# Kernel optimization log

Measured on AMD Instinct MI355X. Metric: run time of the kernel, lower is better.

The kernel has to match this reference:

```python
import jax, jax.numpy as jnp
import numpy as np

D_MODEL = 768
D_STATE = 128
D_CONV = 4
EXPAND = 4
D_INNER = EXPAND * D_MODEL  # 3072
DT_RANK = 48  # ceil(768/16), mamba default dt_rank='auto'
H_MLP = 768
EPS = 1e-6


def setup_inputs() -> dict:
    key = jax.random.key(0)
    ks = jax.random.split(key, 12)
    B, T = 1, 384

    def rn(k, shape, s=0.02):
        return jax.random.normal(k, shape, jnp.float32) * s

    inp = {}
    inp["x"] = jax.random.normal(ks[0], (B, 3 * T, D_MODEL), jnp.float32)
    inp["ln_w"] = jnp.ones((6, D_MODEL), jnp.float32)  # ln1..ln6 RMSNorm weights
    # 3 independent Mamba blocks, params stacked on leading dim
    inp["in_proj_w"] = rn(ks[1], (3, 2 * D_INNER, D_MODEL))
    inp["conv_w"] = rn(ks[2], (3, D_INNER, 1, D_CONV), 0.1)  # depthwise causal conv1d
    inp["conv_b"] = rn(ks[3], (3, D_INNER), 0.1)
    inp["x_proj_w"] = rn(ks[4], (3, DT_RANK + 2 * D_STATE, D_INNER))
    inp["dt_proj_w"] = rn(ks[5], (3, D_INNER, DT_RANK), 0.1)
    inp["dt_proj_b"] = rn(ks[6], (3, D_INNER), 0.1) - 4.0  # small dt after softplus
    A = jnp.tile(jnp.arange(1, D_STATE + 1, dtype=jnp.float32)[None, None, :], (3, D_INNER, 1))
    inp["A_log"] = jnp.log(A)  # mamba S4D-real init
    inp["D_skip"] = jnp.ones((3, D_INNER), jnp.float32)
    inp["out_proj_w"] = rn(ks[7], (3, D_MODEL, D_INNER))
    # 3 GatedMLPs: fc1 -> 2*hidden (value, gate), silu gate, fc2 -> out
    inp["fc1_w"] = rn(ks[8], (3, 2 * H_MLP, D_MODEL))
    inp["fc1_b"] = jnp.zeros((3, 2 * H_MLP), jnp.float32)
    inp["fc2_w"] = rn(ks[9], (3, D_MODEL, H_MLP))
    inp["fc2_b"] = jnp.zeros((3, D_MODEL), jnp.float32)
    return inp


def _rmsnorm(x, w):
    v = jnp.mean(jnp.square(x), axis=-1, keepdims=True)
    return x * jax.lax.rsqrt(v + EPS) * w


def _mamba(u, in_w, cw, cb, xp_w, dt_w, dt_b, A_log, D_skip, out_w):
    # u: (B, T, D_MODEL)
    Bsz = u.shape[0]
    xz = u @ in_w.T  # (B,T,2*Di)
    x, z = jnp.split(xz, 2, axis=-1)
    # causal depthwise conv1d over time
    xc = jax.lax.conv_general_dilated(
        jnp.swapaxes(x, 1, 2), cw, (1,), [(D_CONV - 1, 0)],
        feature_group_count=D_INNER)  # (B,Di,T)
    x = jax.nn.silu(jnp.swapaxes(xc, 1, 2) + cb)  # (B,T,Di)
    x_dbl = x @ xp_w.T  # (B,T,dt_rank+2N)
    dt = x_dbl[..., :DT_RANK]
    Bm = x_dbl[..., DT_RANK:DT_RANK + D_STATE]
    Cm = x_dbl[..., DT_RANK + D_STATE:]
    delta = jax.nn.softplus(dt @ dt_w.T + dt_b)  # (B,T,Di)
    A = -jnp.exp(A_log)  # (Di,N)

    def step(h, inp):
        d_t, B_t, C_t, u_t = inp  # (B,Di),(B,N),(B,N),(B,Di)
        h = jnp.exp(d_t[:, :, None] * A) * h + (d_t * u_t)[:, :, None] * B_t[:, None, :]
        y = jnp.einsum('bdn,bn->bd', h, C_t)
        return h, y

    h0 = jnp.zeros((Bsz, D_INNER, D_STATE), u.dtype)
    xs = tuple(jnp.swapaxes(a, 0, 1) for a in (delta, Bm, Cm, x))  # time-major
    _, ys = jax.lax.scan(jax.checkpoint(step), h0, xs)
    y = jnp.swapaxes(ys, 0, 1) + x * D_skip  # (B,T,Di)
    return (y * jax.nn.silu(z)) @ out_w.T  # (B,T,D_MODEL)


def _gmlp(x, w1, b1, w2, b2):
    h = x @ w1.T + b1
    a, g = jnp.split(h, 2, axis=-1)
    return (jax.nn.silu(g) * a) @ w2.T + b2


def reference(x, ln_w, in_proj_w, conv_w, conv_b, x_proj_w, dt_proj_w, dt_proj_b,
              A_log, D_skip, out_proj_w, fc1_w, fc1_b, fc2_w, fc2_b):
    t = x.shape[1] // 3
    outs = []
    for i in range(3):  # music / up / down branches
        b = x[:, i * t:(i + 1) * t]
        b = b + _mamba(_rmsnorm(b, ln_w[2 * i]), in_proj_w[i], conv_w[i], conv_b[i],
                       x_proj_w[i], dt_proj_w[i], dt_proj_b[i], A_log[i], D_skip[i],
                       out_proj_w[i])
        b = b + _gmlp(_rmsnorm(b, ln_w[2 * i + 1]), fc1_w[i], fc1_b[i], fc2_w[i], fc2_b[i])
        outs.append(b)
    return jnp.concatenate(outs, axis=1)
```

## Files before the change

### kernel.cpp

```cpp
#include <hip/hip_runtime.h>
#include <hip/hip_bf16.h>

#define TSEQ 384
#define DMODEL 768
#define DINNER 3072
#define DSTATE 128
#define DTRANK 48
#define XPROJ_N (DTRANK + 2*DSTATE)
#define NSEG 3
#define LOG2E 1.44269504088896340736f
#define LN2F  0.69314718055994530942f

typedef __attribute__((ext_vector_type(8))) short short8;
typedef __attribute__((ext_vector_type(4))) float floatx4;
typedef unsigned short u16;
typedef unsigned int u32;

__device__ __forceinline__ float bf2f(u16 u) {
    return __uint_as_float(((unsigned)u) << 16);
}
__device__ __forceinline__ float ldf(const void* p, size_t i, int bf) {
    return bf ? bf2f(((const u16*)p)[i]) : ((const float*)p)[i];
}
__device__ __forceinline__ void stf(void* p, size_t i, float v, int bf) {
    if (bf) ((__hip_bfloat16*)p)[i] = __float2bfloat16(v);
    else    ((float*)p)[i] = v;
}
__device__ __forceinline__ float silu_f(float v) { return v / (1.f + __expf(-v)); }
__device__ __forceinline__ u16 f2bf(float f) {
    unsigned u = __float_as_uint(f);
    return (u16)((u + 0x7FFFu + ((u >> 16) & 1u)) >> 16);
}

__device__ __forceinline__ float exp2_fast(float x) {
#if __has_builtin(__builtin_amdgcn_exp2f)
    return __builtin_amdgcn_exp2f(x);
#else
    return exp2f(x);
#endif
}

template<int CTRL>
__device__ __forceinline__ float ror_add(float x) {
    int r = __builtin_amdgcn_update_dpp(0, __float_as_int(x), CTRL, 0xF, 0xF, true);
    return x + __int_as_float(r);
}

__device__ __forceinline__ void gl16(const void* g, void* l) {
    __builtin_amdgcn_global_load_lds(
        (const __attribute__((address_space(1))) u32*)g,
        (__attribute__((address_space(3))) u32*)l, 16, 0, 0);
}

__global__ void k_detect(const unsigned* lnw_bits, int* flag) {
    if (threadIdx.x == 0) {
        flag[0] = (lnw_bits[0] == 0x3F803F80u) ? 1 : 0;
    }
}

__global__ __launch_bounds__(256) void k_rmsnorm(
    const void* src, int src_is_f32, const void* lnw, int wbase,
    u16* out, const int* flagp)
{
    int bf  = *flagp;
    int sbf = src_is_f32 ? 0 : bf;
    int r   = blockIdx.x;
    int seg = r / TSEQ;
    int wrow = 2*seg + wbase;
    int tid = threadIdx.x;
    float v[3]; float s = 0.f;
    #pragma unroll
    for (int j = 0; j < 3; ++j) {
        int e = j*256 + tid;
        v[j] = ldf(src, (size_t)r*DMODEL + e, sbf);
        s += v[j]*v[j];
    }
    __shared__ float red[256];
    red[tid] = s; __syncthreads();
    for (int st = 128; st > 0; st >>= 1) {
        if (tid < st) red[tid] += red[tid+st];
        __syncthreads();
    }
    float rs = rsqrtf(red[0]/(float)DMODEL + 1e-6f);
    #pragma unroll
    for (int j = 0; j < 3; ++j) {
        int e = j*256 + tid;
        out[(size_t)r*DMODEL + e] = f2bf(v[j]*rs*ldf(lnw, (size_t)wrow*DMODEL + e, bf));
    }
}

__global__ __launch_bounds__(256) void k_gemm(
    const float* A, const void* W, const void* bias,
    float* C, const int* flagp, int M, int N, int K, int lda)
{
    int bf  = *flagp;
    int seg = blockIdx.z;
    int mbase = blockIdx.y * 64, nbase = blockIdx.x * 64;
    int tid = threadIdx.x;
    int tx = tid & 15, ty = tid >> 4;

    __shared__ float As[16][68];
    __shared__ float Ws[16][68];

    const float* Ag = A + (size_t)seg*M*lda;
    size_t segW = (size_t)seg*N*K;

    int lrow = tid >> 2;
    int lk   = (tid & 3) * 4;
    int wn   = nbase + lrow;

    float acc[4][4];
    #pragma unroll
    for (int i = 0; i < 4; ++i)
        #pragma unroll
        for (int j = 0; j < 4; ++j) acc[i][j] = 0.f;

    for (int kt = 0; kt < K; kt += 16) {
        float4 av = *reinterpret_cast<const float4*>(Ag + (size_t)(mbase+lrow)*lda + kt + lk);
        As[lk+0][lrow] = av.x; As[lk+1][lrow] = av.y;
        As[lk+2][lrow] = av.z; As[lk+3][lrow] = av.w;
        float w0=0.f, w1=0.f, w2=0.f, w3=0.f;
        if (wn < N) {
            size_t off = segW + (size_t)wn*K + kt + lk;
            if (bf) {
                ushort4 q = *reinterpret_cast<const ushort4*>((const u16*)W + off);
                w0 = bf2f(q.x); w1 = bf2f(q.y); w2 = bf2f(q.z); w3 = bf2f(q.w);
            } else {
                float4 f = *reinterpret_cast<const float4*>((const float*)W + off);
                w0 = f.x; w1 = f.y; w2 = f.z; w3 = f.w;
            }
        }
        Ws[lk+0][lrow] = w0; Ws[lk+1][lrow] = w1;
        Ws[lk+2][lrow] = w2; Ws[lk+3][lrow] = w3;
        __syncthreads();
        #pragma unroll
        for (int kk = 0; kk < 16; ++kk) {
            float4 a4 = *reinterpret_cast<const float4*>(&As[kk][ty*4]);
            float4 b4 = *reinterpret_cast<const float4*>(&Ws[kk][tx*4]);
            float ar[4] = {a4.x, a4.y, a4.z, a4.w};
            float br[4] = {b4.x, b4.y, b4.z, b4.w};
            #pragma unroll
            for (int i = 0; i < 4; ++i)
                #pragma unroll
                for (int j = 0; j < 4; ++j)
                    acc[i][j] = fmaf(ar[i], br[j], acc[i][j]);
        }
        __syncthreads();
    }

    #pragma unroll
    for (int i = 0; i < 4; ++i) {
        int m = mbase + ty*4 + i;
        #pragma unroll
        for (int j = 0; j < 4; ++j) {
            int n = nbase + tx*4 + j;
            if (n < N) {
                float v = acc[i][j] + ldf(bias, (size_t)seg*N + n, bf);
                v = (v > 20.f) ? v : log1pf(__expf(v));
                C[((size_t)(seg*M + m))*N + n] = v;
            }
        }
    }
}

__global__ __launch_bounds__(256) void k_gemm_mfma64g(
    const u16* A, const void* W, const void* bias, const void* resid,
    int resid_flagged, void* C, int c_mode, const int* flagp,
    int M, int N, int K, int ksplit)
{
    int bf  = *flagp;
    int zz  = blockIdx.z;
    int seg = zz / ksplit, ks = zz - seg*ksplit;
    int mbase = blockIdx.y * 64, nbase = blockIdx.x * 64;
    int tid = threadIdx.x;
    int w = tid >> 6, lane = tid & 63;
    int wm = w >> 1, wn = w & 1;
    int quad = lane >> 4, l16 = lane & 15;

    __shared__ short As[3][64*64];
    __shared__ short Ws[3][64*64];

    int nk = (K >> 6) / ksplit;
    size_t k0 = ((size_t)ks * nk) << 6;
    const u16* Ag = A + (size_t)seg*M*K + (size_t)mbase*K + k0;
    size_t segWK = (size_t)seg*N*K;

    int srow = lane >> 3;
    int scol = ((lane & 7) ^ srow) * 8;
    int swz  = (l16 & 7) * 8;

    floatx4 acc[2][2];
    #pragma unroll
    for (int i = 0; i < 2; ++i)
        #pragma unroll
        for (int j = 0; j < 2; ++j)
            acc[i][j] = (floatx4){0.f, 0.f, 0.f, 0.f};

    auto CMP = [&](int b) {
        #pragma unroll
        for (int kk = 0; kk < 2; ++kk) {
            short8 af[2], bfr[2];
            #pragma unroll
            for (int i = 0; i < 2; ++i) {
                int row = wm*32 + i*16 + l16;
                af[i] = *reinterpret_cast<const short8*>(
                    &As[b][row*64 + (((kk*4 + quad)*8) ^ swz)]);
            }
            #pragma unroll
            for (int j = 0; j < 2; ++j) {
                int row = wn*32 + j*16 + l16;
                bfr[j] = *reinterpret_cast<const short8*>(
                    &Ws[b][row*64 + (((kk*4 + quad)*8) ^ swz)]);
            }
            #pragma unroll
            for (int i = 0; i < 2; ++i)
                #pragma unroll
                for (int j = 0; j < 2; ++j)
                    acc[i][j] = __builtin_amdgcn_mfma_f32_16x16x32_bf16(af[i], bfr[j], acc[i][j], 0, 0, 0);
        }
    };

    if (bf) {
        const u16* Wb = (const u16*)W;
        auto STG = [&](int t, int b) {
            size_t kt = (size_t)t << 6;
            #pragma unroll
            for (int i8 = 0; i8 < 2; ++i8) {
                int rbase = w*16 + i8*8;
                gl16(Ag + (size_t)(rbase + srow)*K + kt + scol, &As[b][rbase*64]);
                int wr = nbase + rbase + srow;
                if (wr > N - 1) wr = N - 1;
                gl16(Wb + segWK + (size_t)wr*K + k0 + kt + scol, &Ws[b][rbase*64]);
            }
        };
        STG(0, 0);
        STG(1, 1);
        for (int t = 0; t < nk - 2; ++t) {
            STG(t + 2, (t + 2) % 3);
            asm volatile("s_waitcnt vmcnt(8)" ::: "memory");
            __builtin_amdgcn_s_barrier();
            __builtin_amdgcn_sched_barrier(0);
            CMP(t % 3);
            asm volatile("" ::: "memory");
            __builtin_amdgcn_s_barrier();
        }
        asm volatile("s_waitcnt vmcnt(4)" ::: "memory");
        __builtin_amdgcn_s_barrier();
        __builtin_amdgcn_sched_barrier(0);
        CMP((nk - 2) % 3);
        asm volatile("" ::: "memory");
        __builtin_amdgcn_s_barrier();
        asm volatile("s_waitcnt vmcnt(0)" ::: "memory");
        __builtin_amdgcn_s_barrier();
        __builtin_amdgcn_sched_barrier(0);
        CMP((nk - 1) % 3);
    } else {
        const float* Wf = (const float*)W + segWK;
        int row2 = tid >> 2;
        int wr2 = nbase + row2; if (wr2 > N - 1) wr2 = N - 1;
        for (int t = 0; t < nk; ++t) {
            size_t kt = (size_t)t << 6;
            #pragma unroll
            for (int i8 = 0; i8 < 2; ++i8) {
                int rbase = w*16 + i8*8;
                gl16(Ag + (size_t)(rbase + srow)*K + kt + scol, &As[0][rbase*64]);
            }
            const float* wp = Wf + (size_t)wr2*K + k0 + kt;
            #pragma unroll
            for (int h2 = 0; h2 < 2; ++h2) {
                int gs = (tid & 3) + h2*4;
                short8 s;
                #pragma unroll
                for (int q2 = 0; q2 < 8; ++q2) s[q2] = (short)f2bf(wp[gs*8 + q2]);
                *reinterpret_cast<short8*>(&Ws[0][row2*64 + ((gs ^ (row2 & 7)) * 8)]) = s;
            }
            __syncthreads();
            CMP(0);
            __syncthreads();
        }
    }

    #pragma unroll
    for (int i = 0; i < 2; ++i) {
        #pragma unroll
        for (int reg = 0; reg < 4; ++reg) {
            int grow = mbase + wm*32 + i*16 + quad*4 + reg;
            #pragma unroll
            for (int j = 0; j < 2; ++j) {
                int gcol = nbase + wn*32 + j*16 + l16;
                if (gcol < N) {
                    float v = acc[i][j][reg];
                    size_t idx = ((size_t)(seg*M + grow))*N + gcol;
                    if (ksplit == 1) {
                        if (bias) v += ldf(bias, (size_t)seg*N + gcol, bf);
                        if (resid) v += resid_flagged ? ldf(resid, idx, bf)
                                                      : ((const float*)resid)[idx];
                        if      (c_mode == 0) ((float*)C)[idx] = v;
                        else if (c_mode == 1) ((u16*)C)[idx] = f2bf(v);
                        else                  stf(C, idx, v, bf);
                    } else {
                        if (ks == 0) {
                            if (bias)  v += ldf(bias, (size_t)seg*N + gcol, bf);
                            if (resid) v += resid_flagged ? ldf(resid, idx, bf)
                                                          : ((const float*)resid)[idx];
                        }
                        atomicAdd(&((float*)C)[idx], v);
                    }
                }
            }
        }
    }
}

__global__ __launch_bounds__(256) void k_fc1_gate_g(
    const u16* A, const void* W, const void* bias, u16* act, const int* flagp)
{
    const int M = TSEQ, K = DMODEL, NF = 2*DMODEL;
    int bf  = *flagp;
    int seg = blockIdx.z;
    int mbase = blockIdx.y * 64, nbase = blockIdx.x * 64;
    int tid = threadIdx.x;
    int w = tid >> 6, lane = tid & 63;
    int wm = w >> 1, wn = w & 1;
    int quad = lane >> 4, l16 = lane & 15;

    __shared__ short As[2][64*64];
    __shared__ short Wa[2][64*64];
    __shared__ short Wg[2][64*64];

    const u16* Ag  = A + (size_t)seg*M*K + (size_t)mbase*K;
    const u16* Wap = (const u16*)W + (size_t)seg*NF*K + (size_t)nbase*K;
    const u16* Wgp = Wap + (size_t)DMODEL*K;
    int nk = K >> 6;

    int srow = lane >> 3;
    int scol = ((lane & 7) ^ srow) * 8;
    int swz  = (l16 & 7) * 8;

    floatx4 acca[2][2], accg[2][2];
    #pragma unroll
    for (int i = 0; i < 2; ++i)
        #pragma unroll
        for (int j = 0; j < 2; ++j) {
            acca[i][j] = (floatx4){0.f, 0.f, 0.f, 0.f};
            accg[i][j] = (floatx4){0.f, 0.f, 0.f, 0.f};
        }

    auto CMP = [&](int b) {
        #pragma unroll
        for (int kk = 0; kk < 2; ++kk) {
            short8 af[2], ba[2], bg[2];
            #pragma unroll
            for (int i = 0; i < 2; ++i) {
                int row = wm*32 + i*16 + l16;
                af[i] = *reinterpret_cast<const short8*>(
                    &As[b][row*64 + (((kk*4 + quad)*8) ^ swz)]);
            }
            #pragma unroll
            for (int j = 0; j < 2; ++j) {
                int row = wn*32 + j*16 + l16;
                int col = ((kk*4 + quad)*8) ^ swz;
                ba[j] = *reinterpret_cast<const short8*>(&Wa[b][row*64 + col]);
                bg[j] = *reinterpret_cast<const short8*>(&Wg[b][row*64 + col]);
            }
            #pragma unroll
            for (int i = 0; i < 2; ++i)
                #pragma unroll
                for (int j = 0; j < 2; ++j) {
                    acca[i][j] = __builtin_amdgcn_mfma_f32_16x16x32_bf16(af[i], ba[j], acca[i][j], 0, 0, 0);
                    accg[i][j] = __builtin_amdgcn_mfma_f32_16x16x32_bf16(af[i], bg[j], accg[i][j], 0, 0, 0);
                }
        }
    };

    if (bf) {
        auto STG = [&](int t, int b) {
            size_t kt = (size_t)t << 6;
            #pragma unroll
            for (int i8 = 0; i8 < 2; ++i8) {
                int rbase = w*16 + i8*8;
                size_t so = (size_t)(rbase + srow)*K + kt + scol;
                gl16(Ag  + so, &As[b][rbase*64]);
                gl16(Wap + so, &Wa[b][rbase*64]);
                gl16(Wgp + so, &Wg[b][rbase*64]);
            }
        };
        STG(0, 0);
        for (int t = 0; t < nk - 1; ++t) {
            STG(t + 1, (t + 1) & 1);
            asm volatile("s_waitcnt vmcnt(6)" ::: "memory");
            __builtin_amdgcn_s_barrier();
            __builtin_amdgcn_sched_barrier(0);
            CMP(t & 1);
            asm volatile("" ::: "memory");
            __builtin_amdgcn_s_barrier();
        }
        asm volatile("s_waitcnt vmcnt(0)" ::: "memory");
        __builtin_amdgcn_s_barrier();
        __builtin_amdgcn_sched_barrier(0);
        CMP((nk - 1) & 1);
    } else {
        const float* Waf = (const float*)W + (size_t)seg*NF*K + (size_t)nbase*K;
        const float* Wgf = Waf + (size_t)DMODEL*K;
        int row2 = tid >> 2;
        for (int t = 0; t < nk; ++t) {
            size_t kt = (size_t)t << 6;
            #pragma unroll
            for (int i8 = 0; i8 < 2; ++i8) {
                int rbase = w*16 + i8*8;
                gl16(Ag + (size_t)(rbase + srow)*K + kt + scol, &As[0][rbase*64]);
            }
            #pragma unroll
            for (int h2 = 0; h2 < 2; ++h2) {
                int gs = (tid & 3) + h2*4;
                int wcol = (gs ^ (row2 & 7)) * 8;
                short8 sa, sg;
                const float* wpa = Waf + (size_t)row2*K + kt + gs*8;
                const float* wpg = Wgf + (size_t)row2*K + kt + gs*8;
                #pragma unroll
                for (int q2 = 0; q2 < 8; ++q2) { sa[q2] = (short)f2bf(wpa[q2]); sg[q2] = (short)f2bf(wpg[q2]); }
                *reinterpret_cast<short8*>(&Wa[0][row2*64 + wcol]) = sa;
                *reinterpret_cast<short8*>(&Wg[0][row2*64 + wcol]) = sg;
            }
            __syncthreads();
            CMP(0);
            __syncthreads();
        }
    }

    #pragma unroll
    for (int i = 0; i < 2; ++i) {
        #pragma unroll
        for (int reg = 0; reg < 4; ++reg) {
            int grow = mbase + wm*32 + i*16 + quad*4 + reg;
            #pragma unroll
            for (int j = 0; j < 2; ++j) {
                int gcol = nbase + wn*32 + j*16 + l16;
                float va = acca[i][j][reg] + ldf(bias, (size_t)seg*NF + gcol, bf);
                float vg = accg[i][j][reg] + ldf(bias, (size_t)seg*NF + DMODEL + gcol, bf);
                act[((size_t)(seg*M + grow))*DMODEL + gcol] = f2bf(va * silu_f(vg));
            }
        }
    }
}

__global__ __launch_bounds__(256) void k_conv(
    const u16* xz, const void* cw, const void* cb, u16* xconv, const int* flagp)
{
    int bf = *flagp;
    size_t gid = ((size_t)blockIdx.x*256 + threadIdx.x) * 8;
    int d = (int)(gid % DINNER);
    size_t rt = gid / DINNER;
    int t = (int)(rt % TSEQ);
    int seg = (int)(rt / TSEQ);

    float wv[4][8];
    if (bf) {
        const u16* cwp = (const u16*)cw + ((size_t)seg*DINNER + d)*4;
        #pragma unroll
        for (int q = 0; q < 4; ++q) {
            short8 s = *reinterpret_cast<const short8*>(cwp + q*8);
            #pragma unroll
            for (int e = 0; e < 8; ++e) {
                int idx = q*8 + e;
                wv[idx & 3][idx >> 2] = bf2f((u16)s[e]);
            }
        }
    } else {
        const float* cwp = (const float*)cw + ((size_t)seg*DINNER + d)*4;
        #pragma unroll
        for (int idx = 0; idx < 32; ++idx)
            wv[idx & 3][idx >> 2] = cwp[idx];
    }

    float acc[8];
    #pragma unroll
    for (int e = 0; e < 8; ++e) acc[e] = ldf(cb, (size_t)seg*DINNER + d + e, bf);

    const u16* xs = xz + (size_t)seg*TSEQ*(2*DINNER) + d;
    #pragma unroll
    for (int j = 0; j < 4; ++j) {
        int ts = t - 3 + j;
        if (ts >= 0) {
            short8 v = *reinterpret_cast<const short8*>(xs + (size_t)ts*(2*DINNER));
            #pragma unroll
            for (int e = 0; e < 8; ++e)
                acc[e] = fmaf(wv[j][e], bf2f((u16)v[e]), acc[e]);
        }
    }
    short8 o;
    #pragma unroll
    for (int e = 0; e < 8; ++e) o[e] = (short)f2bf(silu_f(acc[e]));
    *reinterpret_cast<short8*>(xconv + gid) = o;
}

#define WSCH 4
#define WSCT 8
#define NPAIR (TSEQ/(2*WSCT))
#define NBX   (DINNER/WSCH)
#define GUARD_TH 0.04f

__global__ __launch_bounds__(64) void k_scan_wave(
    const float* delta, const u16* xconv, const float* xdbl, const u16* xz,
    const void* A_log, const void* D_skip, u16* yout, const int* flagp)
{
    int bf   = flagp[0];
    int seg  = blockIdx.y;
    int bx = (int)blockIdx.x;
    bx = (bx & 7) * (NBX/8) + (bx >> 3);
    int dbase = bx * WSCH;
    int lane = threadIdx.x;
    int ch = lane >> 4, sl = lane & 15;
    int d = dbase + ch;

    __shared__ float4 BUF[2][WSCT][64];
    __shared__ float  DLB2[WSCT][8];

    float a[8];
    size_t abase = ((size_t)seg*DINNER + d)*DSTATE + (size_t)sl*8;
    #pragma unroll
    for (int j = 0; j < 8; ++j)
        a[j] = -__expf(ldf(A_log, abase + j, bf)) * LOG2E;
    float gl[8]; float gmax = 0.f;
    gl[0] = 0.f;
    #pragma unroll
    for (int j = 1; j < 8; ++j) {
        gl[j] = (a[j] - a[j-1]) * LN2F;
        gmax = fmaxf(gmax, fabsf(gl[j]));
    }
    float wg = gmax;
    #pragma unroll
    for (int k = 32; k >= 1; k >>= 1) wg = fmaxf(wg, __shfl_xor(wg, k));
    float a0  = a[0];
    float Dsk = ldf(D_skip, (size_t)seg*DINNER + d, bf);
    float dskg = (sl == 0) ? Dsk : 0.f;

    const float* xdbl_s = xdbl + (size_t)seg*TSEQ*XPROJ_N;
    int loff = DTRANK + (lane & 15)*8 + ((lane >> 4) & 1)*4 + ((lane >> 5) ? DSTATE : 0);
    const float* srcl = xdbl_s + loff;

    const float* delta_s = delta + (size_t)seg*TSEQ*DINNER + dbase;
    const u16*   xconv_s = xconv + (size_t)seg*TSEQ*DINNER + dbase;
    const u16*   z_s     = xz    + (size_t)seg*TSEQ*(2*DINNER) + DINNER + dbase + ch;
    u16*         y_s     = yout  + (size_t)seg*TSEQ*DINNER + dbase + ch;

    float4  pdel = (float4){0.f, 0.f, 0.f, 0.f};
    ushort4 pu   = (ushort4){0, 0, 0, 0};
    u16     pz   = 0;

    auto STAGE = [&](int tile, int buf) {
        const float* rb = srcl + (size_t)tile*WSCT*XPROJ_N;
        #pragma unroll
        for (int t = 0; t < WSCT; ++t)
            gl16(rb + (size_t)t*XPROJ_N, &BUF[buf][t][0]);
    };
    auto PLOAD = [&](int tile) {
        if (lane < WSCT) {
            size_t ro = (size_t)(tile*WSCT + lane)*DINNER;
            pdel = *reinterpret_cast<const float4*>(delta_s + ro);
            pu   = *reinterpret_cast<const ushort4*>(xconv_s + ro);
        }
    };
    auto DSTORE = [&]() -> bool {
        if (lane < WSCT) {
            float4 w0 = (float4){pdel.x, bf2f(pu.x), pdel.y, bf2f(pu.y)};
            float4 w1 = (float4){pdel.z, bf2f(pu.z), pdel.w, bf2f(pu.w)};
            *reinterpret_cast<float4*>(&DLB2[lane][0]) = w0;
            *reinterpret_cast<float4*>(&DLB2[lane][4]) = w1;
        }
        float m4 = fmaxf(fmaxf(pdel.x, pdel.y), fmaxf(pdel.z, pdel.w));
        return __any(m4 * wg > GUARD_TH);
    };

    float h[8];
    #pragma unroll
    for (int j = 0; j < 8; ++j) h[j] = 0.f;
    float yr = 0.f;

    float2 duA, duB, duC;
    float4 b0A, b1A, c0A, c1A;
    float4 b0B, b1B, c0B, c1B;
    float4 b0C, b1C, c0C, c1C;

#define LOADOPS(BP, T, S) do {                                                \
    du##S = *reinterpret_cast<const float2*>(&DLB2[T][ch*2]);                 \
    b0##S = (BP)[(T)*64 + sl];                                                \
    b1##S = (BP)[(T)*64 + 16 + sl];                                           \
    c0##S = (BP)[(T)*64 + 32 + sl];                                           \
    c1##S = (BP)[(T)*64 + 48 + sl];                                           \
} while (0)

#define COMPUTE(S, T) do {                                                    \
    float del = du##S.x, ut = du##S.y;                                        \
    float duu = del * ut;                                                     \
    float e0,e1,e2,e3,e4,e5,e6,e7;                                            \
    if (gf) {                                                                 \
        e0 = exp2_fast(del * a0);                                             \
        e1 = e0 * fmaf(del, gl[1], 1.f);                                      \
        e2 = e1 * fmaf(del, gl[2], 1.f);                                      \
        e3 = e2 * fmaf(del, gl[3], 1.f);                                      \
        e4 = e3 * fmaf(del, gl[4], 1.f);                                      \
        e5 = e4 * fmaf(del, gl[5], 1.f);                                      \
        e6 = e5 * fmaf(del, gl[6], 1.f);                                      \
        e7 = e6 * fmaf(del, gl[7], 1.f);                                      \
    } else {                                                                  \
        e0 = exp2_fast(del*a[0]); e1 = exp2_fast(del*a[1]);                   \
        e2 = exp2_fast(del*a[2]); e3 = exp2_fast(del*a[3]);                   \
        e4 = exp2_fast(del*a[4]); e5 = exp2_fast(del*a[5]);                   \
        e6 = exp2_fast(del*a[6]); e7 = exp2_fast(del*a[7]);                   \
    }                                                                         \
    h[0] = fmaf(e0, h[0], duu*b0##S.x);                                       \
    h[1] = fmaf(e1, h[1], duu*b0##S.y);                                       \
    h[2] = fmaf(e2, h[2], duu*b0##S.z);                                       \
    h[3] = fmaf(e3, h[3], duu*b0##S.w);                                       \
    h[4] = fmaf(e4, h[4], duu*b1##S.x);                                       \
    h[5] = fmaf(e5, h[5], duu*b1##S.y);                                       \
    h[6] = fmaf(e6, h[6], duu*b1##S.z);                                       \
    h[7] = fmaf(e7, h[7], duu*b1##S.w);                                       \
    float p0 = ut * dskg;                                                     \
    p0 = fmaf(h[0], c0##S.x, p0);                                             \
    p0 = fmaf(h[1], c0##S.y, p0);                                             \
    p0 = fmaf(h[2], c0##S.z, p0);                                             \
    p0 = fmaf(h[3], c0##S.w, p0);                                             \
    float p1 = h[4]*c1##S.x;                                                  \
    p1 = fmaf(h[5], c1##S.y, p1);                                             \
    p1 = fmaf(h[6], c1##S.z, p1);                                             \
    p1 = fmaf(h[7], c1##S.w, p1);                                             \
    float p = p0 + p1;                                                        \
    p = ror_add<0x128>(p);                                                    \
    p = ror_add<0x124>(p);                                                    \
    p = ror_add<0x122>(p);                                                    \
    p = ror_add<0x121>(p);                                                    \
    if (sl == (half8 | (T))) yr = p;                                          \
} while (0)

    auto do_tile = [&](const float4* bp, bool gf, int half8) {
        LOADOPS(bp, 0, A);
        LOADOPS(bp, 1, B);
        LOADOPS(bp, 2, C);
        COMPUTE(A, 0);
        LOADOPS(bp, 3, A);
        COMPUTE(B, 1);
        LOADOPS(bp, 4, B);
        COMPUTE(C, 2);
        LOADOPS(bp, 5, C);
        COMPUTE(A, 3);
        LOADOPS(bp, 6, A);
        COMPUTE(B, 4);
        LOADOPS(bp, 7, B);
        COMPUTE(C, 5);
        COMPUTE(A, 6);
        COMPUTE(B, 7);
    };

    STAGE(0, 0);
    PLOAD(0);

    for (int p = 0; p < NPAIR; ++p) {
        int tA = 2*p;
        asm volatile("s_waitcnt vmcnt(0)" ::: "memory");
        bool exA = DSTORE();
        STAGE(tA + 1, 1);
        PLOAD(tA + 1);
        pz = z_s[(size_t)(p*16 + sl) * (size_t)(2*DINNER)];
        __builtin_amdgcn_sched_barrier(0);
        do_tile(&BUF[0][0][0], !exA, 0);
        asm volatile("s_waitcnt vmcnt(0)" ::: "memory");
        bool exB = DSTORE();
        if (tA + 2 < 2*NPAIR) {
            STAGE(tA + 2, 0);
            PLOAD(tA + 2);
        }
        __builtin_amdgcn_sched_barrier(0);
        do_tile(&BUF[1][0][0], !exB, 8);
        y_s[(size_t)(p*16 + sl) * (size_t)DINNER] = f2bf(yr * silu_f(bf2f(pz)));
        yr = 0.f;
    }
#undef LOADOPS
#undef COMPUTE
}

extern "C" void kernel_launch(void* const* d_in, const int* in_sizes, int n_in,
                              void* d_out, int out_size, void* d_ws, size_t ws_size,
                              hipStream_t stream) {
    const void* x     = d_in[0];
    const void* lnw   = d_in[1];
    const void* inw   = d_in[2];
    const void* convw = d_in[3];
    const void* convb = d_in[4];
    const void* xpw   = d_in[5];
    const void* dtw   = d_in[6];
    const void* dtb   = d_in[7];
    const void* alog  = d_in[8];
    const void* dsk   = d_in[9];
    const void* outw  = d_in[10];
    const void* fc1w  = d_in[11];
    const void* fc1b  = d_in[12];
    const void* fc2w  = d_in[13];
    const void* fc2b  = d_in[14];

    int* flag = (int*)d_ws;
    char* wsb = (char*)d_ws;
    const size_t N_U    = (size_t)NSEG*TSEQ*DMODEL;
    const size_t N_XZ   = (size_t)NSEG*TSEQ*2*DINNER;
    const size_t N_XC   = (size_t)NSEG*TSEQ*DINNER;
    const size_t N_XDBL = (size_t)NSEG*TSEQ*XPROJ_N;

    u16*   u     = (u16*)(wsb + 16);
    u16*   xz    = u + N_U;
    u16*   xconv = xz + N_XZ;
    float* xdbl  = (float*)(xconv + N_XC);
    float* delta = xdbl + N_XDBL;
    u16*   yfin  = (u16*)(delta + N_XC);
    float* b1    = (float*)(yfin + N_XC);
    u16*   actb  = (u16*)(b1 + N_U);

    k_detect<<<1, 64, 0, stream>>>((const unsigned*)lnw, flag);
    hipMemsetAsync(xdbl, 0, N_XDBL*sizeof(float), stream);
    hipMemsetAsync(b1,   0, N_U*sizeof(float),   stream);

    k_rmsnorm<<<NSEG*TSEQ, 256, 0, stream>>>(x, 0, lnw, 0, u, flag);
    k_gemm_mfma64g<<<dim3(96, 6, NSEG), 256, 0, stream>>>(u, inw, nullptr, nullptr, 0,
        xz, 1, flag, TSEQ, 2*DINNER, DMODEL, 1);
    k_conv<<<(NSEG*TSEQ*DINNER)/(256*8), 256, 0, stream>>>(xz, convw, convb, xconv, flag);
    k_gemm_mfma64g<<<dim3(5, 6, NSEG*4), 256, 0, stream>>>(xconv, xpw, nullptr, nullptr, 0,
        xdbl, 0, flag, TSEQ, XPROJ_N, DINNER, 4);
    k_gemm<<<dim3(48, 6, NSEG), 256, 0, stream>>>(xdbl, dtw, dtb,
        delta, flag, TSEQ, DINNER, DTRANK, XPROJ_N);

    k_scan_wave<<<dim3(NBX, NSEG), 64, 0, stream>>>(
        delta, xconv, xdbl, xz, alog, dsk, yfin, flag);

    k_gemm_mfma64g<<<dim3(12, 6, NSEG*4), 256, 0, stream>>>(yfin, outw, nullptr, x, 1,
        b1, 0, flag, TSEQ, DMODEL, DINNER, 4);

    k_rmsnorm<<<NSEG*TSEQ, 256, 0, stream>>>(b1, 1, lnw, 1, u, flag);
    k_fc1_gate_g<<<dim3(12, 6, NSEG), 256, 0, stream>>>(u, fc1w, fc1b, actb, flag);
    k_gemm_mfma64g<<<dim3(12, 6, NSEG), 256, 0, stream>>>(actb, fc2w, fc2b, b1, 0,
        d_out, 2, flag, TSEQ, DMODEL, DMODEL, 1);
}
```

Baseline: 496.0 us.

## Split scan wave over 2 channels with 4 states per lane and swizzle reduction

The selective-scan wave kernel now handles 2 channels per 64-lane wave instead of 4. Each lane owns 4 states instead of 8, over 4-step time tiles. The per-step cross-lane reduction grows from 4 DPP row-rotate adds to 5 ds_swizzle adds spanning 32 lanes. This shortens each lane's serial per-step work and doubles the number of waves, at the cost of more blocks, a longer reduction built on LDS-path swizzles, and more sync points per sequence.

Result: slower. 522.5 us (+5.4%).

```diff
diff --git a/kernel.cpp b/kernel.cpp
--- a/kernel.cpp
+++ b/kernel.cpp
@@ -40,9 +40,9 @@
 #endif
 }
 
-template<int CTRL>
-__device__ __forceinline__ float ror_add(float x) {
-    int r = __builtin_amdgcn_update_dpp(0, __float_as_int(x), CTRL, 0xF, 0xF, true);
+template<int MASK>
+__device__ __forceinline__ float swz_add(float x) {
+    int r = __builtin_amdgcn_ds_swizzle(__float_as_int(x), MASK);
     return x + __int_as_float(r);
 }
 
@@ -494,8 +494,8 @@
     *reinterpret_cast<short8*>(xconv + gid) = o;
 }
 
-#define WSCH 4
-#define WSCT 8
+#define WSCH 2
+#define WSCT 4
 #define NPAIR (TSEQ/(2*WSCT))
 #define NBX   (DINNER/WSCH)
 #define GUARD_TH 0.04f
@@ -510,21 +510,22 @@
     bx = (bx & 7) * (NBX/8) + (bx >> 3);
     int dbase = bx * WSCH;
     int lane = threadIdx.x;
-    int ch = lane >> 4, sl = lane & 15;
+    int ch = lane >> 5, sl = lane & 31;
     int d = dbase + ch;
+    int bq = (sl & 1)*16 + (sl >> 1);
 
     __shared__ float4 BUF[2][WSCT][64];
-    __shared__ float  DLB2[WSCT][8];
-
-    float a[8];
-    size_t abase = ((size_t)seg*DINNER + d)*DSTATE + (size_t)sl*8;
-    #pragma unroll
-    for (int j = 0; j < 8; ++j)
+    __shared__ float  DLB2[WSCT][4];
+
+    float a[4];
+    size_t abase = ((size_t)seg*DINNER + d)*DSTATE + (size_t)sl*4;
+    #pragma unroll
+    for (int j = 0; j < 4; ++j)
         a[j] = -__expf(ldf(A_log, abase + j, bf)) * LOG2E;
-    float gl[8]; float gmax = 0.f;
+    float gl[4]; float gmax = 0.f;
     gl[0] = 0.f;
     #pragma unroll
-    for (int j = 1; j < 8; ++j) {
+    for (int j = 1; j < 4; ++j) {
         gl[j] = (a[j] - a[j-1]) * LN2F;
         gmax = fmaxf(gmax, fabsf(gl[j]));
     }
@@ -544,9 +545,9 @@
     const u16*   z_s     = xz    + (size_t)seg*TSEQ*(2*DINNER) + DINNER + dbase + ch;
     u16*         y_s     = yout  + (size_t)seg*TSEQ*DINNER + dbase + ch;
 
-    float4  pdel = (float4){0.f, 0.f, 0.f, 0.f};
-    ushort4 pu   = (ushort4){0, 0, 0, 0};
-    u16     pz   = 0;
+    float2 pdel2 = (float2){0.f, 0.f};
+    u32    pu2   = 0;
+    u16    pz    = 0;
 
     auto STAGE = [&](int tile, int buf) {
         const float* rb = srcl + (size_t)tile*WSCT*XPROJ_N;
@@ -557,100 +558,72 @@
     auto PLOAD = [&](int tile) {
         if (lane < WSCT) {
             size_t ro = (size_t)(tile*WSCT + lane)*DINNER;
-            pdel = *reinterpret_cast<const float4*>(delta_s + ro);
-            pu   = *reinterpret_cast<const ushort4*>(xconv_s + ro);
+            pdel2 = *reinterpret_cast<const float2*>(delta_s + ro);
+            pu2   = *reinterpret_cast<const u32*>(xconv_s + ro);
         }
     };
     auto DSTORE = [&]() -> bool {
         if (lane < WSCT) {
-            float4 w0 = (float4){pdel.x, bf2f(pu.x), pdel.y, bf2f(pu.y)};
-            float4 w1 = (float4){pdel.z, bf2f(pu.z), pdel.w, bf2f(pu.w)};
+            float4 w0 = (float4){pdel2.x, bf2f((u16)(pu2 & 0xFFFFu)),
+                                 pdel2.y, bf2f((u16)(pu2 >> 16))};
             *reinterpret_cast<float4*>(&DLB2[lane][0]) = w0;
-            *reinterpret_cast<float4*>(&DLB2[lane][4]) = w1;
-        }
-        float m4 = fmaxf(fmaxf(pdel.x, pdel.y), fmaxf(pdel.z, pdel.w));
-        return __any(m4 * wg > GUARD_TH);
+        }
+        float m2 = fmaxf(pdel2.x, pdel2.y);
+        return __any(m2 * wg > GUARD_TH);
     };
 
-    float h[8];
-    #pragma unroll
-    for (int j = 0; j < 8; ++j) h[j] = 0.f;
+    float h[4];
+    #pragma unroll
+    for (int j = 0; j < 4; ++j) h[j] = 0.f;
     float yr = 0.f;
 
-    float2 duA, duB, duC;
-    float4 b0A, b1A, c0A, c1A;
-    float4 b0B, b1B, c0B, c1B;
-    float4 b0C, b1C, c0C, c1C;
+    float2 duA, duB;
+    float4 bA, cA, bB, cB;
 
 #define LOADOPS(BP, T, S) do {                                                \
     du##S = *reinterpret_cast<const float2*>(&DLB2[T][ch*2]);                 \
-    b0##S = (BP)[(T)*64 + sl];                                                \
-    b1##S = (BP)[(T)*64 + 16 + sl];                                           \
-    c0##S = (BP)[(T)*64 + 32 + sl];                                           \
-    c1##S = (BP)[(T)*64 + 48 + sl];                                           \
+    b##S  = (BP)[(T)*64 + bq];                                                \
+    c##S  = (BP)[(T)*64 + 32 + bq];                                           \
 } while (0)
 
 #define COMPUTE(S, T) do {                                                    \
     float del = du##S.x, ut = du##S.y;                                        \
     float duu = del * ut;                                                     \
-    float e0,e1,e2,e3,e4,e5,e6,e7;                                            \
+    float e0,e1,e2,e3;                                                        \
     if (gf) {                                                                 \
         e0 = exp2_fast(del * a0);                                             \
         e1 = e0 * fmaf(del, gl[1], 1.f);                                      \
         e2 = e1 * fmaf(del, gl[2], 1.f);                                      \
         e3 = e2 * fmaf(del, gl[3], 1.f);                                      \
-        e4 = e3 * fmaf(del, gl[4], 1.f);                                      \
-        e5 = e4 * fmaf(del, gl[5], 1.f);                                      \
-        e6 = e5 * fmaf(del, gl[6], 1.f);                                      \
-        e7 = e6 * fmaf(del, gl[7], 1.f);                                      \
     } else {                                                                  \
         e0 = exp2_fast(del*a[0]); e1 = exp2_fast(del*a[1]);                   \
         e2 = exp2_fast(del*a[2]); e3 = exp2_fast(del*a[3]);                   \
-        e4 = exp2_fast(del*a[4]); e5 = exp2_fast(del*a[5]);                   \
-        e6 = exp2_fast(del*a[6]); e7 = exp2_fast(del*a[7]);                   \
     }                                                                         \
-    h[0] = fmaf(e0, h[0], duu*b0##S.x);                                       \
-    h[1] = fmaf(e1, h[1], duu*b0##S.y);                                       \
-    h[2] = fmaf(e2, h[2], duu*b0##S.z);                                       \
-    h[3] = fmaf(e3, h[3], duu*b0##S.w);                                       \
-    h[4] = fmaf(e4, h[4], duu*b1##S.x);                                       \
-    h[5] = fmaf(e5, h[5], duu*b1##S.y);                                       \
-    h[6] = fmaf(e6, h[6], duu*b1##S.z);                                       \
-    h[7] = fmaf(e7, h[7], duu*b1##S.w);                                       \
-    float p0 = ut * dskg;                                                     \
-    p0 = fmaf(h[0], c0##S.x, p0);                                             \
-    p0 = fmaf(h[1], c0##S.y, p0);                                             \
-    p0 = fmaf(h[2], c0##S.z, p0);                                             \
-    p0 = fmaf(h[3], c0##S.w, p0);                                             \
-    float p1 = h[4]*c1##S.x;                                                  \
-    p1 = fmaf(h[5], c1##S.y, p1);                                             \
-    p1 = fmaf(h[6], c1##S.z, p1);                                             \
-    p1 = fmaf(h[7], c1##S.w, p1);                                             \
-    float p = p0 + p1;                                                        \
-    p = ror_add<0x128>(p);                                                    \
-    p = ror_add<0x124>(p);                                                    \
-    p = ror_add<0x122>(p);                                                    \
-    p = ror_add<0x121>(p);                                                    \
-    if (sl == (half8 | (T))) yr = p;                                          \
+    h[0] = fmaf(e0, h[0], duu*b##S.x);                                        \
+    h[1] = fmaf(e1, h[1], duu*b##S.y);                                        \
+    h[2] = fmaf(e2, h[2], duu*b##S.z);                                        \
+    h[3] = fmaf(e3, h[3], duu*b##S.w);                                        \
+    float p = fmaf(h[0], c##S.x, ut*dskg);                                    \
+    p = fmaf(h[1], c##S.y, p);                                                \
+    p = fmaf(h[2], c##S.z, p);                                                \
+    p = fmaf(h[3], c##S.w, p);                                                \
+    p = swz_add<0x041F>(p);                                       \
+    p = swz_add<0x081F>(p);                                       \
+    p = swz_add<0x101F>(p);                                       \
+    p = swz_add<0x201F>(p);                                       \
+    p = swz_add<0x401F>(p);                                       \
+    if (sl == (half4 | (T))) yr = p;                                          \
 } while (0)
 
-    auto do_tile = [&](const float4* bp, bool gf, int half8) {
+    auto do_tile = [&](const float4* bp, bool gf, int half4) {
         LOADOPS(bp, 0, A);
         LOADOPS(bp, 1, B);
-        LOADOPS(bp, 2, C);
         COMPUTE(A, 0);
-        LOADOPS(bp, 3, A);
+        LOADOPS(bp, 2, A);
         COMPUTE(B, 1);
-        LOADOPS(bp, 4, B);
-        COMPUTE(C, 2);
-        LOADOPS(bp, 5, C);
-        COMPUTE(A, 3);
-        LOADOPS(bp, 6, A);
-        COMPUTE(B, 4);
-        LOADOPS(bp, 7, B);
-        COMPUTE(C, 5);
-        COMPUTE(A, 6);
-        COMPUTE(B, 7);
+        LOADOPS(bp, 3, B);
+        COMPUTE(A, 2);
+        COMPUTE(B, 3);
     };
 
     STAGE(0, 0);
@@ -662,7 +635,7 @@
         bool exA = DSTORE();
         STAGE(tA + 1, 1);
         PLOAD(tA + 1);
-        pz = z_s[(size_t)(p*16 + sl) * (size_t)(2*DINNER)];
+        if (sl < 8) pz = z_s[(size_t)(p*8 + sl) * (size_t)(2*DINNER)];
         __builtin_amdgcn_sched_barrier(0);
         do_tile(&BUF[0][0][0], !exA, 0);
         asm volatile("s_waitcnt vmcnt(0)" ::: "memory");
@@ -672,8 +645,9 @@
             PLOAD(tA + 2);
         }
         __builtin_amdgcn_sched_barrier(0);
-        do_tile(&BUF[1][0][0], !exB, 8);
-        y_s[(size_t)(p*16 + sl) * (size_t)DINNER] = f2bf(yr * silu_f(bf2f(pz)));
+        do_tile(&BUF[1][0][0], !exB, 4);
+        if (sl < 8)
+            y_s[(size_t)(p*8 + sl) * (size_t)DINNER] = f2bf(yr * silu_f(bf2f(pz)));
         yr = 0.f;
     }
 #undef LOADOPS
```
